# Performance work log

Hardware: AMD Instinct MI355X
Metric: run time of the kernel (lower is better)

Reference implementation:

```python
import jax, jax.numpy as jnp
import numpy as np

N, T, V, CIN, COUT = 64, 12, 256, 64, 64


def _conv1x1(h, w, b):
    # h: [n,c,v,w], w: [o,c] (1x1 conv kernel squeezed), b: [o]
    return jnp.einsum('ncvw,oc->novw', h, w) + b[None, :, None, None]


def setup_inputs() -> dict:
    key = jax.random.key(0)
    ks = jax.random.split(key, 8)
    x = jax.random.normal(ks[0], (N, CIN, T, V), jnp.float32)
    feats = jax.random.normal(ks[1], (N, 7, V, V), jnp.float32)
    mask = (jax.random.uniform(ks[2], (N, 1, V, V)) < 0.3).astype(jnp.float32)
    A = jnp.concatenate([feats, mask], axis=1)  # [N, 8, V, V]
    init = lambda k, shape, fan: jax.random.normal(k, shape, jnp.float32) / np.sqrt(fan).astype(np.float32)
    conv_w = init(ks[3], (COUT, CIN), CIN)
    conv_b = jnp.zeros((COUT,), jnp.float32)
    w1 = init(ks[4], (16, 7), 7)
    b1 = jnp.zeros((16,), jnp.float32)
    w2 = init(ks[5], (32, 16), 16)
    b2 = jnp.zeros((32,), jnp.float32)
    w3 = init(ks[6], (64, 32), 32)
    b3 = jnp.zeros((64,), jnp.float32)
    return dict(x=x, A=A, conv_w=conv_w, conv_b=conv_b,
                w1=w1, b1=b1, w2=w2, b2=b2, w3=w3, b3=b3)


def reference(x, A, conv_w, conv_b, w1, b1, w2, b2, w3, b3):
    # 1x1 temporal conv on node features: [n,cin,t,v] -> [n,cout,t,v]
    x = jnp.einsum('nctv,oc->notv', x, conv_w) + conv_b[None, :, None, None]
    mask = A[:, 7:]          # [n,1,v,v]
    h = A[:, :7]             # [n,7,v,v]
    # adjmatder MLP (dropout is identity at inference)
    h = jax.nn.relu(_conv1x1(h, w1, b1))
    h = jax.nn.relu(_conv1x1(h, w2, b2))
    h = jax.nn.relu(_conv1x1(h, w3, b3))   # [n,64,v,v]
    Aw = h * mask
    # per-channel graph convolution: [n,c,t,v] x [n,c,v,w] -> [n,c,t,w]
    out = jnp.einsum('nctv,ncvw->nctw', x, Aw)
    return out, Aw
```

## Files before the change

kernel.cpp:

```cpp
#include <hip/hip_runtime.h>
#include <hip/hip_bf16.h>

#define NB   64
#define TT   12
#define VV   256
#define CIN  64
#define COUT 64
#define VSQ  65536

__global__ __launch_bounds__(256) void k1_conv(
    const float* __restrict__ x, const float* __restrict__ w,
    const float* __restrict__ b, float* __restrict__ y)
{
    const int nt = blockIdx.x;
    const int n  = nt / TT;
    const int t  = nt % TT;
    const int v  = threadIdx.x;

    const float* xp = x + ((long)n * CIN * TT + t) * VV + v;
    float xv[CIN];
    #pragma unroll 8
    for (int c = 0; c < CIN; ++c)
        xv[c] = xp[(long)c * TT * VV];

    float* yp = y + ((long)n * COUT * TT + t) * VV + v;

    for (int o0 = 0; o0 < COUT; o0 += 16) {
        float acc[16];
        #pragma unroll
        for (int i = 0; i < 16; ++i) acc[i] = b[o0 + i];
        #pragma unroll 8
        for (int c = 0; c < CIN; ++c) {
            const float xc = xv[c];
            #pragma unroll
            for (int i = 0; i < 16; ++i)
                acc[i] += w[(o0 + i) * CIN + c] * xc;
        }
        #pragma unroll
        for (int i = 0; i < 16; ++i)
            yp[(long)(o0 + i) * TT * VV] = acc[i];
    }
}

__global__ __launch_bounds__(256) void k2_mlp(
    const float* __restrict__ A,
    const float* __restrict__ w1, const float* __restrict__ b1,
    const float* __restrict__ w2, const float* __restrict__ b2,
    const float* __restrict__ w3, const float* __restrict__ b3,
    float* __restrict__ Aw)
{
    __shared__ float s1[16 * 8];
    __shared__ float sb1[16];
    __shared__ float s2[32 * 16];
    __shared__ float sb2[32];
    __shared__ float s3[64 * 32];
    __shared__ float sb3[64];

    const int tid = threadIdx.x;

    if (tid < 128) s1[tid] = ((tid & 7) < 7) ? w1[(tid >> 3) * 7 + (tid & 7)] : 0.f;
    else if (tid < 144) sb1[tid - 128] = b1[tid - 128];
    else if (tid < 176) sb2[tid - 144] = b2[tid - 144];
    else if (tid < 240) sb3[tid - 176] = b3[tid - 176];
    for (int i = tid; i < 512;  i += 256) s2[i] = w2[i];
    for (int i = tid; i < 2048; i += 256) s3[i] = w3[i];
    __syncthreads();

    const long base = (long)blockIdx.x * 512;
    const int  n    = (int)(base >> 16);
    const int  rem  = ((int)(base & (VSQ - 1))) + 2 * tid;

    const float* ap = A + ((long)n * 8 << 16) + rem;
    float fa[8], fb[8];
    #pragma unroll
    for (int c = 0; c < 7; ++c) {
        const float2 f2 = *reinterpret_cast<const float2*>(ap + ((long)c << 16));
        fa[c] = f2.x; fb[c] = f2.y;
    }
    fa[7] = 0.f; fb[7] = 0.f;
    const float2 m = *reinterpret_cast<const float2*>(ap + ((long)7 << 16));

    float h1a[16], h1b[16];
    #pragma unroll
    for (int o = 0; o < 16; ++o) {
        float a = sb1[o], bb = a;
        #pragma unroll
        for (int k4 = 0; k4 < 8; k4 += 4) {
            const float4 wv = *reinterpret_cast<const float4*>(&s1[o * 8 + k4]);
            a  += wv.x * fa[k4] + wv.y * fa[k4 + 1] + wv.z * fa[k4 + 2] + wv.w * fa[k4 + 3];
            bb += wv.x * fb[k4] + wv.y * fb[k4 + 1] + wv.z * fb[k4 + 2] + wv.w * fb[k4 + 3];
        }
        h1a[o] = fmaxf(a, 0.f); h1b[o] = fmaxf(bb, 0.f);
    }

    float h2a[32], h2b[32];
    #pragma unroll
    for (int o = 0; o < 32; ++o) {
        float a = sb2[o], bb = a;
        #pragma unroll
        for (int k4 = 0; k4 < 16; k4 += 4) {
            const float4 wv = *reinterpret_cast<const float4*>(&s2[o * 16 + k4]);
            a  += wv.x * h1a[k4] + wv.y * h1a[k4 + 1] + wv.z * h1a[k4 + 2] + wv.w * h1a[k4 + 3];
            bb += wv.x * h1b[k4] + wv.y * h1b[k4 + 1] + wv.z * h1b[k4 + 2] + wv.w * h1b[k4 + 3];
        }
        h2a[o] = fmaxf(a, 0.f); h2b[o] = fmaxf(bb, 0.f);
    }

    float* op = Aw + ((long)n * COUT << 16) + rem;
    for (int o0 = 0; o0 < 64; o0 += 8) {
        float accA[8], accB[8];
        #pragma unroll
        for (int i = 0; i < 8; ++i) { accA[i] = sb3[o0 + i]; accB[i] = accA[i]; }
        #pragma unroll
        for (int k4 = 0; k4 < 32; k4 += 4) {
            #pragma unroll
            for (int i = 0; i < 8; ++i) {
                const float4 wv = *reinterpret_cast<const float4*>(&s3[(o0 + i) * 32 + k4]);
                accA[i] += wv.x * h2a[k4] + wv.y * h2a[k4 + 1] + wv.z * h2a[k4 + 2] + wv.w * h2a[k4 + 3];
                accB[i] += wv.x * h2b[k4] + wv.y * h2b[k4 + 1] + wv.z * h2b[k4 + 2] + wv.w * h2b[k4 + 3];
            }
        }
        #pragma unroll
        for (int i = 0; i < 8; ++i) {
            float2 r;
            r.x = fmaxf(accA[i], 0.f) * m.x;
            r.y = fmaxf(accB[i], 0.f) * m.y;
            *reinterpret_cast<float2*>(op + ((long)(o0 + i) << 16)) = r;
        }
    }
}

__global__ __launch_bounds__(256) void k3_einsum(
    const float* __restrict__ Aw, const float* __restrict__ y,
    float* __restrict__ out)
{
    __shared__ float ys[4][TT][VV];

    const int n   = blockIdx.x >> 4;
    const int c0  = (blockIdx.x & 15) * 4;
    const int tid = threadIdx.x;
    const int cq  = tid >> 6;
    const int w4  = (tid & 63) * 4;

    {
        const float* src = y + ((long)(n * COUT + c0) * TT) * VV;
        float* dst = &ys[0][0][0];
        #pragma unroll
        for (int it = 0; it < 12; ++it) {
            const int idx = tid + it * 256;
            *reinterpret_cast<float4*>(dst + idx * 4) =
                *reinterpret_cast<const float4*>(src + idx * 4);
        }
    }
    __syncthreads();

    const float* awp = Aw + (((long)(n * COUT + c0 + cq)) << 16) + w4;
    float4 acc[TT];
    #pragma unroll
    for (int t = 0; t < TT; ++t) acc[t] = make_float4(0.f, 0.f, 0.f, 0.f);

    #pragma unroll 2
    for (int v = 0; v < VV; ++v) {
        const float4 aw = *reinterpret_cast<const float4*>(awp + (long)v * VV);
        #pragma unroll
        for (int t = 0; t < TT; ++t) {
            const float xs = ys[cq][t][v];
            acc[t].x += xs * aw.x;
            acc[t].y += xs * aw.y;
            acc[t].z += xs * aw.z;
            acc[t].w += xs * aw.w;
        }
    }

    float* op = out + ((long)(n * COUT + c0 + cq) * TT) * VV + w4;
    #pragma unroll
    for (int t = 0; t < TT; ++t)
        *reinterpret_cast<float4*>(op + t * VV) = acc[t];
}

extern "C" void kernel_launch(void* const* d_in, const int* in_sizes, int n_in,
                              void* d_out, int out_size, void* d_ws, size_t ws_size,
                              hipStream_t stream)
{
    const float* x      = (const float*)d_in[0];
    const float* A      = (const float*)d_in[1];
    const float* conv_w = (const float*)d_in[2];
    const float* conv_b = (const float*)d_in[3];
    const float* w1     = (const float*)d_in[4];
    const float* b1     = (const float*)d_in[5];
    const float* w2     = (const float*)d_in[6];
    const float* b2     = (const float*)d_in[7];
    const float* w3     = (const float*)d_in[8];
    const float* b3     = (const float*)d_in[9];

    float* out = (float*)d_out;
    float* Aw  = (float*)d_out + (long)NB * COUT * TT * VV;
    const size_t y_bytes = (size_t)NB * COUT * TT * VV * sizeof(float);

    float* y = (ws_size >= y_bytes) ? (float*)d_ws : out;

    k2_mlp<<<(NB * VSQ) / 512, 256, 0, stream>>>(A, w1, b1, w2, b2, w3, b3, Aw);

    k1_conv<<<NB * TT, 256, 0, stream>>>(x, conv_w, conv_b, y);

    k3_einsum<<<NB * (COUT / 4), 256, 0, stream>>>(Aw, y, out);
}
```

Before: 717.7 us.

## Read MLP weights directly from global memory and vectorize einsum shared loads

The MLP kernel no longer stages weights and biases in shared memory with a barrier. It reads them straight from global memory as uniform, read-only values, which the compiler can turn into scalar loads, and it restructures the output-channel blocking. The einsum kernel now loads four v-values per float4 from shared memory and unrolls four Aw rows per step, cutting LDS instruction count at the cost of more registers. The launch order of the conv and MLP kernels is also swapped.

```diff
diff --git a/kernel.cpp b/kernel.cpp
--- a/kernel.cpp
+++ b/kernel.cpp
@@ -49,82 +49,81 @@
     const float* __restrict__ w3, const float* __restrict__ b3,
     float* __restrict__ Aw)
 {
-    __shared__ float s1[16 * 8];
-    __shared__ float sb1[16];
-    __shared__ float s2[32 * 16];
-    __shared__ float sb2[32];
-    __shared__ float s3[64 * 32];
-    __shared__ float sb3[64];
-
-    const int tid = threadIdx.x;
-
-    if (tid < 128) s1[tid] = ((tid & 7) < 7) ? w1[(tid >> 3) * 7 + (tid & 7)] : 0.f;
-    else if (tid < 144) sb1[tid - 128] = b1[tid - 128];
-    else if (tid < 176) sb2[tid - 144] = b2[tid - 144];
-    else if (tid < 240) sb3[tid - 176] = b3[tid - 176];
-    for (int i = tid; i < 512;  i += 256) s2[i] = w2[i];
-    for (int i = tid; i < 2048; i += 256) s3[i] = w3[i];
-    __syncthreads();
-
+    const int  tid  = threadIdx.x;
     const long base = (long)blockIdx.x * 512;
     const int  n    = (int)(base >> 16);
     const int  rem  = ((int)(base & (VSQ - 1))) + 2 * tid;
 
     const float* ap = A + ((long)n * 8 << 16) + rem;
-    float fa[8], fb[8];
+    float fa[7], fb[7];
     #pragma unroll
     for (int c = 0; c < 7; ++c) {
         const float2 f2 = *reinterpret_cast<const float2*>(ap + ((long)c << 16));
         fa[c] = f2.x; fb[c] = f2.y;
     }
-    fa[7] = 0.f; fb[7] = 0.f;
     const float2 m = *reinterpret_cast<const float2*>(ap + ((long)7 << 16));
 
     float h1a[16], h1b[16];
-    #pragma unroll
-    for (int o = 0; o < 16; ++o) {
-        float a = sb1[o], bb = a;
-        #pragma unroll
-        for (int k4 = 0; k4 < 8; k4 += 4) {
-            const float4 wv = *reinterpret_cast<const float4*>(&s1[o * 8 + k4]);
-            a  += wv.x * fa[k4] + wv.y * fa[k4 + 1] + wv.z * fa[k4 + 2] + wv.w * fa[k4 + 3];
-            bb += wv.x * fb[k4] + wv.y * fb[k4 + 1] + wv.z * fb[k4 + 2] + wv.w * fb[k4 + 3];
-        }
-        h1a[o] = fmaxf(a, 0.f); h1b[o] = fmaxf(bb, 0.f);
+    {
+        float aA[16], aB[16];
+        #pragma unroll
+        for (int i = 0; i < 16; ++i) { aA[i] = b1[i]; aB[i] = aA[i]; }
+        #pragma unroll
+        for (int k = 0; k < 7; ++k) {
+            #pragma unroll
+            for (int i = 0; i < 16; ++i) {
+                const float wv = w1[i * 7 + k];
+                aA[i] += wv * fa[k];
+                aB[i] += wv * fb[k];
+            }
+        }
+        #pragma unroll
+        for (int i = 0; i < 16; ++i) {
+            h1a[i] = fmaxf(aA[i], 0.f);
+            h1b[i] = fmaxf(aB[i], 0.f);
+        }
     }
 
     float h2a[32], h2b[32];
-    #pragma unroll
-    for (int o = 0; o < 32; ++o) {
-        float a = sb2[o], bb = a;
-        #pragma unroll
-        for (int k4 = 0; k4 < 16; k4 += 4) {
-            const float4 wv = *reinterpret_cast<const float4*>(&s2[o * 16 + k4]);
-            a  += wv.x * h1a[k4] + wv.y * h1a[k4 + 1] + wv.z * h1a[k4 + 2] + wv.w * h1a[k4 + 3];
-            bb += wv.x * h1b[k4] + wv.y * h1b[k4 + 1] + wv.z * h1b[k4 + 2] + wv.w * h1b[k4 + 3];
-        }
-        h2a[o] = fmaxf(a, 0.f); h2b[o] = fmaxf(bb, 0.f);
+    for (int o0 = 0; o0 < 32; o0 += 8) {
+        float aA[8], aB[8];
+        #pragma unroll
+        for (int i = 0; i < 8; ++i) { aA[i] = b2[o0 + i]; aB[i] = aA[i]; }
+        #pragma unroll
+        for (int k = 0; k < 16; ++k) {
+            #pragma unroll
+            for (int i = 0; i < 8; ++i) {
+                const float wv = w2[(o0 + i) * 16 + k];
+                aA[i] += wv * h1a[k];
+                aB[i] += wv * h1b[k];
+            }
+        }
+        #pragma unroll
+        for (int i = 0; i < 8; ++i) {
+            h2a[o0 + i] = fmaxf(aA[i], 0.f);
+            h2b[o0 + i] = fmaxf(aB[i], 0.f);
+        }
     }
 
     float* op = Aw + ((long)n * COUT << 16) + rem;
-    for (int o0 = 0; o0 < 64; o0 += 8) {
-        float accA[8], accB[8];
-        #pragma unroll
-        for (int i = 0; i < 8; ++i) { accA[i] = sb3[o0 + i]; accB[i] = accA[i]; }
-        #pragma unroll
-        for (int k4 = 0; k4 < 32; k4 += 4) {
-            #pragma unroll
-            for (int i = 0; i < 8; ++i) {
-                const float4 wv = *reinterpret_cast<const float4*>(&s3[(o0 + i) * 32 + k4]);
-                accA[i] += wv.x * h2a[k4] + wv.y * h2a[k4 + 1] + wv.z * h2a[k4 + 2] + wv.w * h2a[k4 + 3];
-                accB[i] += wv.x * h2b[k4] + wv.y * h2b[k4 + 1] + wv.z * h2b[k4 + 2] + wv.w * h2b[k4 + 3];
+    for (int o0 = 0; o0 < 64; o0 += 16) {
+        float aA[16], aB[16];
+        #pragma unroll
+        for (int i = 0; i < 16; ++i) { aA[i] = b3[o0 + i]; aB[i] = aA[i]; }
+        #pragma unroll 8
+        for (int k = 0; k < 32; ++k) {
+            #pragma unroll
+            for (int i = 0; i < 16; ++i) {
+                const float wv = w3[(o0 + i) * 32 + k];
+                aA[i] += wv * h2a[k];
+                aB[i] += wv * h2b[k];
             }
         }
         #pragma unroll
-        for (int i = 0; i < 8; ++i) {
+        for (int i = 0; i < 16; ++i) {
             float2 r;
-            r.x = fmaxf(accA[i], 0.f) * m.x;
-            r.y = fmaxf(accB[i], 0.f) * m.y;
+            r.x = fmaxf(aA[i], 0.f) * m.x;
+            r.y = fmaxf(aB[i], 0.f) * m.y;
             *reinterpret_cast<float2*>(op + ((long)(o0 + i) << 16)) = r;
         }
     }
@@ -159,16 +158,23 @@
     #pragma unroll
     for (int t = 0; t < TT; ++t) acc[t] = make_float4(0.f, 0.f, 0.f, 0.f);
 
-    #pragma unroll 2
-    for (int v = 0; v < VV; ++v) {
-        const float4 aw = *reinterpret_cast<const float4*>(awp + (long)v * VV);
+    for (int v0 = 0; v0 < VV; v0 += 4) {
+        float4 xs[TT];
+        #pragma unroll
+        for (int t = 0; t < TT; ++t)
+            xs[t] = *reinterpret_cast<const float4*>(&ys[cq][t][v0]);
+
+        const float4 aw0 = *reinterpret_cast<const float4*>(awp + (long)(v0 + 0) * VV);
+        const float4 aw1 = *reinterpret_cast<const float4*>(awp + (long)(v0 + 1) * VV);
+        const float4 aw2 = *reinterpret_cast<const float4*>(awp + (long)(v0 + 2) * VV);
+        const float4 aw3 = *reinterpret_cast<const float4*>(awp + (long)(v0 + 3) * VV);
+
         #pragma unroll
         for (int t = 0; t < TT; ++t) {
-            const float xs = ys[cq][t][v];
-            acc[t].x += xs * aw.x;
-            acc[t].y += xs * aw.y;
-            acc[t].z += xs * aw.z;
-            acc[t].w += xs * aw.w;
+            acc[t].x += xs[t].x * aw0.x + xs[t].y * aw1.x + xs[t].z * aw2.x + xs[t].w * aw3.x;
+            acc[t].y += xs[t].x * aw0.y + xs[t].y * aw1.y + xs[t].z * aw2.y + xs[t].w * aw3.y;
+            acc[t].z += xs[t].x * aw0.z + xs[t].y * aw1.z + xs[t].z * aw2.z + xs[t].w * aw3.z;
+            acc[t].w += xs[t].x * aw0.w + xs[t].y * aw1.w + xs[t].z * aw2.w + xs[t].w * aw3.w;
         }
     }
 
@@ -199,9 +205,9 @@
 
     float* y = (ws_size >= y_bytes) ? (float*)d_ws : out;
 
+    k1_conv<<<NB * TT, 256, 0, stream>>>(x, conv_w, conv_b, y);
+
     k2_mlp<<<(NB * VSQ) / 512, 256, 0, stream>>>(A, w1, b1, w2, b2, w3, b3, Aw);
 
-    k1_conv<<<NB * TT, 256, 0, stream>>>(x, conv_w, conv_b, y);
-
     k3_einsum<<<NB * (COUT / 4), 256, 0, stream>>>(Aw, y, out);
 }
```

New measurement: 714.3 us. Within noise of the previous version (-0.5%).
